# Kernel optimization log

Measured on AMD Instinct MI355X. Metric: run time of the kernel, lower is better.

Reference implementation:

```python
import jax, jax.numpy as jnp
import numpy as np

V, N = 3, 32768
C2, C3 = 256, 32          # feat_ch_2D, feat_ch_3D
H = W = 128               # 2D feature map size
D = 32                    # 3D volume feature size
CIN = C2 + C3             # 288, MLP in_channels


def setup_inputs() -> dict:
    key = jax.random.key(0)
    ks = jax.random.split(key, 16)
    sc = 0.02
    inp = {
        'pts': jax.random.uniform(ks[0], (1, N, 3), minval=-0.5, maxval=0.5),
        'pts_proj': jax.random.uniform(ks[1], (1, N, 2), minval=-1.0, maxval=1.0),
        'img_feat0': jax.random.normal(ks[2], (V, C2, H, W)),
        'img_feat1': jax.random.normal(ks[3], (V, C2, H, W)),
        'vol_feat0': jax.random.normal(ks[4], (V, C3, D, D, D)),
        'vol_feat1': jax.random.normal(ks[5], (V, C3, D, D, D)),
        'W0': jax.random.normal(ks[6], (1024, CIN)) * sc,  'b0': jnp.zeros((1024,)),
        'W1': jax.random.normal(ks[7], (512, CIN + 1024)) * sc, 'b1': jnp.zeros((512,)),
        'W2': jax.random.normal(ks[8], (256, CIN + 512)) * sc,  'b2': jnp.zeros((256,)),
        'W3': jax.random.normal(ks[9], (128, CIN + 256)) * sc,  'b3': jnp.zeros((128,)),
        'W4': jax.random.normal(ks[10], (1, 128)) * sc,         'b4': jnp.zeros((1,)),
        'mean_num': 3,
    }
    return inp


def _gs2d(feat, gx, gy):
    # feat: [C,H,W]; gx,gy: [N] normalized coords in [-1,1]
    C, Hh, Ww = feat.shape
    ix = jnp.clip(((gx + 1.0) * Ww - 1.0) * 0.5, 0.0, Ww - 1.0)  # align_corners=False, border pad
    iy = jnp.clip(((gy + 1.0) * Hh - 1.0) * 0.5, 0.0, Hh - 1.0)
    x0f, y0f = jnp.floor(ix), jnp.floor(iy)
    wx, wy = ix - x0f, iy - y0f
    x0 = x0f.astype(jnp.int32); x1 = jnp.minimum(x0 + 1, Ww - 1)
    y0 = y0f.astype(jnp.int32); y1 = jnp.minimum(y0 + 1, Hh - 1)
    v00 = feat[:, y0, x0]; v01 = feat[:, y0, x1]
    v10 = feat[:, y1, x0]; v11 = feat[:, y1, x1]
    return (v00 * (1 - wy) * (1 - wx) + v01 * (1 - wy) * wx
            + v10 * wy * (1 - wx) + v11 * wy * wx)  # [C,N]


def _gs3d(feat, gx, gy, gz):
    # feat: [C,D,H,W]; grid x->W, y->H, z->D (torch grid_sample convention)
    C, Dd, Hh, Ww = feat.shape
    ix = jnp.clip(((gx + 1.0) * Ww - 1.0) * 0.5, 0.0, Ww - 1.0)
    iy = jnp.clip(((gy + 1.0) * Hh - 1.0) * 0.5, 0.0, Hh - 1.0)
    iz = jnp.clip(((gz + 1.0) * Dd - 1.0) * 0.5, 0.0, Dd - 1.0)
    x0f, y0f, z0f = jnp.floor(ix), jnp.floor(iy), jnp.floor(iz)
    wx, wy, wz = ix - x0f, iy - y0f, iz - z0f
    x0 = x0f.astype(jnp.int32); x1 = jnp.minimum(x0 + 1, Ww - 1)
    y0 = y0f.astype(jnp.int32); y1 = jnp.minimum(y0 + 1, Hh - 1)
    z0 = z0f.astype(jnp.int32); z1 = jnp.minimum(z0 + 1, Dd - 1)
    def g(zi, yi, xi):
        return feat[:, zi, yi, xi]  # [C,N]
    out = (g(z0, y0, x0) * (1 - wz) * (1 - wy) * (1 - wx)
           + g(z0, y0, x1) * (1 - wz) * (1 - wy) * wx
           + g(z0, y1, x0) * (1 - wz) * wy * (1 - wx)
           + g(z0, y1, x1) * (1 - wz) * wy * wx
           + g(z1, y0, x0) * wz * (1 - wy) * (1 - wx)
           + g(z1, y0, x1) * wz * (1 - wy) * wx
           + g(z1, y1, x0) * wz * wy * (1 - wx)
           + g(z1, y1, x1) * wz * wy * wx)
    return out  # [C,N]


def _lrelu(x):
    return jnp.where(x >= 0, x, 0.2 * x)


def _conv1x1(Wm, bm, x):
    # x: [V,C,N] -> [V,O,N]
    return jnp.einsum('oc,vcn->von', Wm, x) + bm[None, :, None]


def _mlp0(x, W0, b0, W1, b1, W2, b2, W3, b3):
    out = _lrelu(_conv1x1(W0, b0, x))
    out = _lrelu(_conv1x1(W1, b1, jnp.concatenate([x, out], axis=1)))
    out = _lrelu(_conv1x1(W2, b2, jnp.concatenate([x, out], axis=1)))
    out = _lrelu(_conv1x1(W3, b3, jnp.concatenate([x, out], axis=1)))
    return out  # [V,128,N]


def _forward(pts, pts_proj, img_feats, vol_feats,
             W0, b0, W1, b1, W2, b2, W3, b3, W4, b4, mean_num):
    v = img_feats[0].shape[0]
    gx2 = jnp.broadcast_to(pts_proj[:, :, 0], (v, pts_proj.shape[1]))
    gy2 = jnp.broadcast_to(pts_proj[:, :, 1], (v, pts_proj.shape[1]))
    p = pts * 2.0  # pts *= 2.0 before 3D sampling
    gx3 = jnp.broadcast_to(p[:, :, 0], (v, p.shape[1]))
    gy3 = jnp.broadcast_to(p[:, :, 1], (v, p.shape[1]))
    gz3 = jnp.broadcast_to(p[:, :, 2], (v, p.shape[1]))
    outs = []
    for img_feat, vol_feat in zip(img_feats, vol_feats):
        f2 = jax.vmap(_gs2d)(img_feat, gx2, gy2)            # [V,C2,N]
        f3 = jax.vmap(_gs3d)(vol_feat, gx3, gy3, gz3)       # [V,C3,N]
        pt_feat = jnp.concatenate([f2, f3], axis=1)         # [V,288,N]
        pt_out0 = _mlp0(pt_feat, W0, b0, W1, b1, W2, b2, W3, b3)
        pt_out0_mean = jnp.mean(pt_out0[:mean_num], axis=0, keepdims=True)  # [1,128,N]
        sdf = jax.nn.sigmoid(_conv1x1(W4, b4, pt_out0_mean))                # [1,1,N]
        outs.append(jnp.transpose(sdf, (0, 2, 1)))                          # [1,N,1]
    return tuple(outs)


def reference(pts, pts_proj, img_feat0, img_feat1, vol_feat0, vol_feat1,
              W0, b0, W1, b1, W2, b2, W3, b3, W4, b4, mean_num):
    return _forward(pts, pts_proj, [img_feat0, img_feat1], [vol_feat0, vol_feat1],
                    W0, b0, W1, b1, W2, b2, W3, b3, W4, b4, mean_num)
```

## Files before the change

### kernel.cpp

```cpp
#include <hip/hip_runtime.h>
#include <hip/hip_bf16.h>

#define NV 3
#define NPTS 32768
#define C2C 256
#define C3C 32
#define CINC 288
#define HH 128
#define WWW 128
#define DDD 32

typedef short bh8 __attribute__((ext_vector_type(8)));
typedef float fx4 __attribute__((ext_vector_type(4)));
typedef unsigned short us4 __attribute__((ext_vector_type(4)));

__device__ __forceinline__ float b2f(unsigned short u) {
    unsigned int x = ((unsigned int)u) << 16;
    return __uint_as_float(x);
}
__device__ __forceinline__ unsigned short f2b(float f) {
    unsigned int x = __float_as_uint(f);
    unsigned int r = (x + 0x7FFFu + ((x >> 16) & 1u)) >> 16;
    return (unsigned short)r;
}

__device__ __forceinline__ void gl2lds16(const unsigned short* g, unsigned short* l) {
    __builtin_amdgcn_global_load_lds(
        (const __attribute__((address_space(1))) unsigned int*)g,
        (__attribute__((address_space(3))) unsigned int*)l, 16, 0, 0);
}

__global__ void k_f2b(const float* __restrict__ src, unsigned short* __restrict__ dst, int n) {
    int i = blockIdx.x * 256 + threadIdx.x;
    if (i < n) dst[i] = f2b(src[i]);
}

__global__ void k_timg(const float* __restrict__ in, unsigned short* __restrict__ out) {
    int v = blockIdx.x >> 7, y = blockIdx.x & 127;
    int x0 = blockIdx.y << 6, c0 = blockIdx.z << 6;
    __shared__ float t[64][65];
    int tx = threadIdx.x & 63, tg = threadIdx.x >> 6;
    const float* src = in + (((size_t)(v * C2C + c0) * HH + y) * WWW + x0);
#pragma unroll
    for (int i = 0; i < 16; i++) {
        int cl = tg * 16 + i;
        t[cl][tx] = src[(size_t)cl * (HH * WWW) + tx];
    }
    __syncthreads();
    unsigned short* dst = out + ((size_t)(v * HH + y) * WWW + x0) * C2C + c0;
#pragma unroll
    for (int i = 0; i < 16; i++) {
        int xl = tg * 16 + i;
        dst[(size_t)xl * C2C + tx] = f2b(t[tx][xl]);
    }
}

__global__ void k_tvol(const float* __restrict__ in, unsigned short* __restrict__ out) {
    int v = blockIdx.x;
    int s0 = blockIdx.y << 8;
    __shared__ float t[32][257];
    int tid = threadIdx.x;
    const float* src = in + (size_t)v * C3C * 32768 + s0;
#pragma unroll
    for (int c = 0; c < 32; c++) t[c][tid] = src[(size_t)c * 32768 + tid];
    __syncthreads();
    unsigned short* dst = out + ((size_t)v * 32768 + s0) * C3C;
    int c = tid & 31, sb = tid >> 5;
#pragma unroll
    for (int j = 0; j < 32; j++) {
        int sl = j * 8 + sb;
        dst[(size_t)sl * C3C + c] = f2b(t[c][sl]);
    }
}

__global__ __launch_bounds__(256) void k_sample(const float* __restrict__ pts, const float* __restrict__ proj,
                         const unsigned short* __restrict__ imgT, const unsigned short* __restrict__ volT,
                         unsigned short* __restrict__ ptT, int n0, int Nk) {
    int w = threadIdx.x >> 6, l = threadIdx.x & 63;
    int i = blockIdx.x * 4 + w;
    int v = blockIdx.y;
    int n = n0 + i;
    unsigned short* dstRow = ptT + (size_t)(v * Nk + i) * CINC;

    {
        float gx = proj[n * 2 + 0], gy = proj[n * 2 + 1];
        float ix = fminf(fmaxf(((gx + 1.0f) * (float)WWW - 1.0f) * 0.5f, 0.0f), (float)(WWW - 1));
        float iy = fminf(fmaxf(((gy + 1.0f) * (float)HH - 1.0f) * 0.5f, 0.0f), (float)(HH - 1));
        float x0f = floorf(ix), y0f = floorf(iy);
        float wx = ix - x0f, wy = iy - y0f;
        int x0 = (int)x0f, y0 = (int)y0f;
        int x1 = min(x0 + 1, WWW - 1), y1 = min(y0 + 1, HH - 1);
        const unsigned short* base = imgT + (size_t)v * HH * WWW * C2C;
        const us4* p00 = (const us4*)(base + ((size_t)(y0 * WWW + x0)) * C2C) + l;
        const us4* p01 = (const us4*)(base + ((size_t)(y0 * WWW + x1)) * C2C) + l;
        const us4* p10 = (const us4*)(base + ((size_t)(y1 * WWW + x0)) * C2C) + l;
        const us4* p11 = (const us4*)(base + ((size_t)(y1 * WWW + x1)) * C2C) + l;
        us4 a = *p00, b = *p01, c = *p10, d = *p11;
        float w00 = (1.0f - wy) * (1.0f - wx), w01 = (1.0f - wy) * wx;
        float w10 = wy * (1.0f - wx), w11 = wy * wx;
        us4 rv;
#pragma unroll
        for (int r = 0; r < 4; r++) {
            float f = b2f(a[r]) * w00 + b2f(b[r]) * w01 + b2f(c[r]) * w10 + b2f(d[r]) * w11;
            rv[r] = f2b(f);
        }
        *(us4*)(dstRow + l * 4) = rv;
    }
    {
        float gx = pts[n * 3 + 0] * 2.0f, gy = pts[n * 3 + 1] * 2.0f, gz = pts[n * 3 + 2] * 2.0f;
        float ix = fminf(fmaxf(((gx + 1.0f) * (float)DDD - 1.0f) * 0.5f, 0.0f), (float)(DDD - 1));
        float iy = fminf(fmaxf(((gy + 1.0f) * (float)DDD - 1.0f) * 0.5f, 0.0f), (float)(DDD - 1));
        float iz = fminf(fmaxf(((gz + 1.0f) * (float)DDD - 1.0f) * 0.5f, 0.0f), (float)(DDD - 1));
        float x0f = floorf(ix), y0f = floorf(iy), z0f = floorf(iz);
        float wx = ix - x0f, wy = iy - y0f, wz = iz - z0f;
        int x0 = (int)x0f, y0 = (int)y0f, z0 = (int)z0f;
        int x1 = min(x0 + 1, DDD - 1), y1 = min(y0 + 1, DDD - 1), z1 = min(z0 + 1, DDD - 1);
        int c = l & 31, zs = l >> 5;
        int zi = zs ? z1 : z0;
        float wzs = zs ? wz : (1.0f - wz);
        const unsigned short* base = volT + (size_t)v * 32768 * C3C;
        float f00 = b2f(base[((size_t)((zi * 32 + y0) * 32 + x0)) * C3C + c]);
        float f01 = b2f(base[((size_t)((zi * 32 + y0) * 32 + x1)) * C3C + c]);
        float f10 = b2f(base[((size_t)((zi * 32 + y1) * 32 + x0)) * C3C + c]);
        float f11 = b2f(base[((size_t)((zi * 32 + y1) * 32 + x1)) * C3C + c]);
        float r = (f00 * (1.0f - wy) * (1.0f - wx) + f01 * (1.0f - wy) * wx +
                   f10 * wy * (1.0f - wx) + f11 * wy * wx) * wzs;
        float other = __shfl_xor(r, 32);
        r += other;
        if (zs == 0) dstRow[C2C + c] = f2b(r);
    }
}

__global__ __launch_bounds__(256) void k_gemm(const unsigned short* __restrict__ A, int K,
                                              const unsigned short* __restrict__ B1, int K1,
                                              const unsigned short* __restrict__ B2, int K2,
                                              const float* __restrict__ bias,
                                              unsigned short* __restrict__ C, int M) {
    __shared__ unsigned short As[128 * 32];
    __shared__ unsigned short Bs[128 * 32];
    int tid = threadIdx.x;
    int w = tid >> 6, l = tid & 63;
    int la = l & 15, lg = l >> 4;
    int wm = w & 1, wn = w >> 1;
    int mBlk = blockIdx.x * 128;
    int nBlk = blockIdx.y * 128;

    int sRow = l >> 2;
    int sCol = (l & 3) * 8;

    fx4 acc[4][4];
#pragma unroll
    for (int mi = 0; mi < 4; mi++)
#pragma unroll
        for (int ni = 0; ni < 4; ni++) acc[mi][ni] = (fx4){0.f, 0.f, 0.f, 0.f};

    const unsigned short* Ag = A + (size_t)mBlk * K;
    const unsigned short* Bg;

#define KLOOP(BPTR, KB, AOFF)                                                                  \
    Bg = (BPTR) + (size_t)nBlk * (KB);                                                         \
    for (int k0 = 0; k0 < (KB); k0 += 32) {                                                    \
        _Pragma("unroll")                                                                      \
        for (int j = 0; j < 2; j++) {                                                          \
            int r = w * 32 + j * 16 + sRow;                                                    \
            gl2lds16(Ag + (size_t)r * K + (AOFF) + k0 + sCol, &As[r * 32 + sCol]);             \
            gl2lds16(Bg + (size_t)r * (KB) + k0 + sCol, &Bs[r * 32 + sCol]);                   \
        }                                                                                      \
        __syncthreads();                                                                       \
        bh8 af[4], bf8[4];                                                                     \
        _Pragma("unroll")                                                                      \
        for (int mi = 0; mi < 4; mi++) af[mi] = *(const bh8*)&As[(wm * 64 + mi * 16 + la) * 32 + lg * 8]; \
        _Pragma("unroll")                                                                      \
        for (int ni = 0; ni < 4; ni++) bf8[ni] = *(const bh8*)&Bs[(wn * 64 + ni * 16 + la) * 32 + lg * 8]; \
        _Pragma("unroll")                                                                      \
        for (int mi = 0; mi < 4; mi++)                                                         \
            _Pragma("unroll")                                                                  \
            for (int ni = 0; ni < 4; ni++)                                                     \
                acc[mi][ni] = __builtin_amdgcn_mfma_f32_16x16x32_bf16(af[mi], bf8[ni], acc[mi][ni], 0, 0, 0); \
        __syncthreads();                                                                       \
    }

    KLOOP(B1, K1, 0)
    if (B2 != nullptr) {
        KLOOP(B2, K2, K1)
    }
#undef KLOOP

#pragma unroll
    for (int mi = 0; mi < 4; mi++) {
        int m0 = mBlk + wm * 64 + mi * 16 + lg * 4;
        fx4 bb = *(const fx4*)(bias + m0);
#pragma unroll
        for (int ni = 0; ni < 4; ni++) {
            int n = nBlk + wn * 64 + ni * 16 + la;
            us4 rv;
#pragma unroll
            for (int r = 0; r < 4; r++) {
                float x = acc[mi][ni][r] + bb[r];
                x = (x >= 0.0f) ? x : 0.2f * x;
                rv[r] = f2b(x);
            }
            *(us4*)(C + (size_t)n * M + m0) = rv;
        }
    }
}

__global__ void k_head(const unsigned short* __restrict__ o3, const float* __restrict__ W4,
                       const float* __restrict__ b4, const int* __restrict__ mn_p,
                       float* __restrict__ out, int n0, int Nk, int level) {
    int i = blockIdx.x * 256 + threadIdx.x;
    if (i >= Nk) return;
    int mn = *mn_p;
    if (mn > NV) mn = NV;
    if (mn < 1) mn = 1;
    float s = 0.0f;
    for (int v = 0; v < mn; v++) {
        const unsigned short* row = o3 + (size_t)(v * Nk + i) * 128;
        for (int c0 = 0; c0 < 128; c0 += 8) {
            bh8 x = *(const bh8*)(row + c0);
#pragma unroll
            for (int r = 0; r < 8; r++) s += W4[c0 + r] * b2f((unsigned short)x[r]);
        }
    }
    s = s / (float)mn + b4[0];
    out[(size_t)level * NPTS + n0 + i] = 1.0f / (1.0f + expf(-s));
}

extern "C" void kernel_launch(void* const* d_in, const int* in_sizes, int n_in,
                              void* d_out, int out_size, void* d_ws, size_t ws_size,
                              hipStream_t stream) {
    const float* pts = (const float*)d_in[0];
    const float* proj = (const float*)d_in[1];
    const float* img[2] = {(const float*)d_in[2], (const float*)d_in[3]};
    const float* vol[2] = {(const float*)d_in[4], (const float*)d_in[5]};
    const float* Wf[4] = {(const float*)d_in[6], (const float*)d_in[8], (const float*)d_in[10], (const float*)d_in[12]};
    const float* bf[4] = {(const float*)d_in[7], (const float*)d_in[9], (const float*)d_in[11], (const float*)d_in[13]};
    const float* W4 = (const float*)d_in[14];
    const float* b4 = (const float*)d_in[15];
    const int* mn = (const int*)d_in[16];
    float* out = (float*)d_out;

    const int Ksz[4] = {288, 1312, 800, 544};
    const int Msz[4] = {1024, 512, 256, 128};

    char* ws = (char*)d_ws;
    size_t off = 0;
    auto alloc = [&](size_t bytes) -> char* {
        char* p = ws + off;
        off = (off + bytes + 255) & ~(size_t)255;
        return p;
    };

    unsigned short* Wb[4];
    for (int i = 0; i < 4; i++) Wb[i] = (unsigned short*)alloc((size_t)Msz[i] * Ksz[i] * 2);
    unsigned short* imgT = (unsigned short*)alloc((size_t)NV * HH * WWW * C2C * 2);
    unsigned short* volT = (unsigned short*)alloc((size_t)NV * 32768 * C3C * 2);
    size_t fixed = off;

    const size_t perPt = (size_t)NV * 2 * (CINC + 1024 + 512 + 256 + 128);
    int Nk = NPTS;
    if (fixed + (size_t)Nk * perPt + 4096 > ws_size) {
        size_t avail = (ws_size > fixed + 4096) ? (ws_size - fixed - 4096) : 0;
        long nk = (long)(avail / perPt);
        nk = (nk / 128) * 128;
        if (nk < 128) nk = 128;
        if (nk > NPTS) nk = NPTS;
        Nk = (int)nk;
    }
    unsigned short* ptT = (unsigned short*)alloc((size_t)NV * Nk * CINC * 2);
    unsigned short* o0 = (unsigned short*)alloc((size_t)NV * Nk * 1024 * 2);
    unsigned short* o1 = (unsigned short*)alloc((size_t)NV * Nk * 512 * 2);
    unsigned short* o2 = (unsigned short*)alloc((size_t)NV * Nk * 256 * 2);
    unsigned short* o3 = (unsigned short*)alloc((size_t)NV * Nk * 128 * 2);

    for (int i = 0; i < 4; i++) {
        int n = Msz[i] * Ksz[i];
        k_f2b<<<(n + 255) / 256, 256, 0, stream>>>(Wf[i], Wb[i], n);
    }

    for (int lvl = 0; lvl < 2; lvl++) {
        k_timg<<<dim3(NV * HH, WWW / 64, C2C / 64), 256, 0, stream>>>(img[lvl], imgT);
        k_tvol<<<dim3(NV, 32768 / 256), 256, 0, stream>>>(vol[lvl], volT);
        for (int n0 = 0; n0 < NPTS; n0 += Nk) {
            int nk = NPTS - n0 < Nk ? NPTS - n0 : Nk;
            int NC = NV * nk;
            k_sample<<<dim3(nk / 4, NV), 256, 0, stream>>>(pts, proj, imgT, volT, ptT, n0, nk);
            k_gemm<<<dim3(1024 / 128, NC / 128), 256, 0, stream>>>(Wb[0], 288, ptT, 288, nullptr, 0, bf[0], o0, 1024);
            k_gemm<<<dim3(512 / 128, NC / 128), 256, 0, stream>>>(Wb[1], 1312, ptT, 288, o0, 1024, bf[1], o1, 512);
            k_gemm<<<dim3(256 / 128, NC / 128), 256, 0, stream>>>(Wb[2], 800, ptT, 288, o1, 512, bf[2], o2, 256);
            k_gemm<<<dim3(128 / 128, NC / 128), 256, 0, stream>>>(Wb[3], 544, ptT, 288, o2, 256, bf[3], o3, 128);
            k_head<<<(nk + 255) / 256, 256, 0, stream>>>(o3, W4, b4, mn, out, n0, nk, lvl);
        }
    }
}
```

Baseline: 1.186 ms.

## Double-buffer GEMM LDS tiles and swizzle workgroups across XCDs

The GEMM kernel now uses two LDS buffers, so loads for the next K-tile are issued before computing on the current one. This halves the barriers per tile and overlaps global-to-LDS transfer with MFMA work. It also remaps block IDs so consecutive tiles land on the same XCD, which should improve L2 reuse. The cost is doubled LDS use per block, which may reduce occupancy.

New measurement: 1.209 ms. About the same (+2.0%).

```diff
diff --git a/kernel.cpp b/kernel.cpp
--- a/kernel.cpp
+++ b/kernel.cpp
@@ -28,6 +28,13 @@
     __builtin_amdgcn_global_load_lds(
         (const __attribute__((address_space(1))) unsigned int*)g,
         (__attribute__((address_space(3))) unsigned int*)l, 16, 0, 0);
+}
+
+__device__ __forceinline__ int xcd_swz(int orig, int nwg) {
+    int xcd = orig & 7;
+    int q = nwg >> 3, r = nwg & 7;
+    int base = (xcd < r) ? xcd * (q + 1) : r * (q + 1) + (xcd - r) * q;
+    return base + (orig >> 3);
 }
 
 __global__ void k_f2b(const float* __restrict__ src, unsigned short* __restrict__ dst, int n) {
@@ -91,11 +98,10 @@
         int x0 = (int)x0f, y0 = (int)y0f;
         int x1 = min(x0 + 1, WWW - 1), y1 = min(y0 + 1, HH - 1);
         const unsigned short* base = imgT + (size_t)v * HH * WWW * C2C;
-        const us4* p00 = (const us4*)(base + ((size_t)(y0 * WWW + x0)) * C2C) + l;
-        const us4* p01 = (const us4*)(base + ((size_t)(y0 * WWW + x1)) * C2C) + l;
-        const us4* p10 = (const us4*)(base + ((size_t)(y1 * WWW + x0)) * C2C) + l;
-        const us4* p11 = (const us4*)(base + ((size_t)(y1 * WWW + x1)) * C2C) + l;
-        us4 a = *p00, b = *p01, c = *p10, d = *p11;
+        us4 a = *((const us4*)(base + ((size_t)(y0 * WWW + x0)) * C2C) + l);
+        us4 b = *((const us4*)(base + ((size_t)(y0 * WWW + x1)) * C2C) + l);
+        us4 c = *((const us4*)(base + ((size_t)(y1 * WWW + x0)) * C2C) + l);
+        us4 d = *((const us4*)(base + ((size_t)(y1 * WWW + x1)) * C2C) + l);
         float w00 = (1.0f - wy) * (1.0f - wx), w01 = (1.0f - wy) * wx;
         float w10 = wy * (1.0f - wx), w11 = wy * wx;
         us4 rv;
@@ -136,17 +142,24 @@
                                               const unsigned short* __restrict__ B2, int K2,
                                               const float* __restrict__ bias,
                                               unsigned short* __restrict__ C, int M) {
-    __shared__ unsigned short As[128 * 32];
-    __shared__ unsigned short Bs[128 * 32];
+    __shared__ unsigned short As0[128 * 32], Bs0[128 * 32];
+    __shared__ unsigned short As1[128 * 32], Bs1[128 * 32];
     int tid = threadIdx.x;
     int w = tid >> 6, l = tid & 63;
     int la = l & 15, lg = l >> 4;
     int wm = w & 1, wn = w >> 1;
-    int mBlk = blockIdx.x * 128;
-    int nBlk = blockIdx.y * 128;
-
-    int sRow = l >> 2;
-    int sCol = (l & 3) * 8;
+    int gx = gridDim.x;
+    int nwg = gx * gridDim.y;
+    int bid = xcd_swz(blockIdx.y * gx + blockIdx.x, nwg);
+    int mBlk = (bid % gx) * 128;
+    int nBlk = (bid / gx) * 128;
+    int sRow = l >> 2, sCol = (l & 3) * 8;
+    int r0 = w * 32 + sRow, r1 = r0 + 16;
+
+    const unsigned short* Ag = A + (size_t)mBlk * K;
+    const unsigned short* B1g = B1 + (size_t)nBlk * K1;
+    const unsigned short* B2g = B2 ? B2 + (size_t)nBlk * K2 : (const unsigned short*)0;
+    int nt1 = K1 >> 5, nt = nt1 + (K2 >> 5);
 
     fx4 acc[4][4];
 #pragma unroll
@@ -154,37 +167,42 @@
 #pragma unroll
         for (int ni = 0; ni < 4; ni++) acc[mi][ni] = (fx4){0.f, 0.f, 0.f, 0.f};
 
-    const unsigned short* Ag = A + (size_t)mBlk * K;
-    const unsigned short* Bg;
-
-#define KLOOP(BPTR, KB, AOFF)                                                                  \
-    Bg = (BPTR) + (size_t)nBlk * (KB);                                                         \
-    for (int k0 = 0; k0 < (KB); k0 += 32) {                                                    \
-        _Pragma("unroll")                                                                      \
-        for (int j = 0; j < 2; j++) {                                                          \
-            int r = w * 32 + j * 16 + sRow;                                                    \
-            gl2lds16(Ag + (size_t)r * K + (AOFF) + k0 + sCol, &As[r * 32 + sCol]);             \
-            gl2lds16(Bg + (size_t)r * (KB) + k0 + sCol, &Bs[r * 32 + sCol]);                   \
-        }                                                                                      \
-        __syncthreads();                                                                       \
-        bh8 af[4], bf8[4];                                                                     \
-        _Pragma("unroll")                                                                      \
-        for (int mi = 0; mi < 4; mi++) af[mi] = *(const bh8*)&As[(wm * 64 + mi * 16 + la) * 32 + lg * 8]; \
-        _Pragma("unroll")                                                                      \
-        for (int ni = 0; ni < 4; ni++) bf8[ni] = *(const bh8*)&Bs[(wn * 64 + ni * 16 + la) * 32 + lg * 8]; \
-        _Pragma("unroll")                                                                      \
-        for (int mi = 0; mi < 4; mi++)                                                         \
-            _Pragma("unroll")                                                                  \
-            for (int ni = 0; ni < 4; ni++)                                                     \
-                acc[mi][ni] = __builtin_amdgcn_mfma_f32_16x16x32_bf16(af[mi], bf8[ni], acc[mi][ni], 0, 0, 0); \
-        __syncthreads();                                                                       \
-    }
-
-    KLOOP(B1, K1, 0)
-    if (B2 != nullptr) {
-        KLOOP(B2, K2, K1)
-    }
-#undef KLOOP
+    auto stage = [&](int t, unsigned short* Asb, unsigned short* Bsb) {
+        const unsigned short* as = Ag + t * 32 + sCol;
+        gl2lds16(as + (size_t)r0 * K, Asb + r0 * 32 + sCol);
+        gl2lds16(as + (size_t)r1 * K, Asb + r1 * 32 + sCol);
+        const unsigned short* bs;
+        size_t ldb;
+        if (t < nt1) { bs = B1g + t * 32 + sCol; ldb = (size_t)K1; }
+        else         { bs = B2g + (t - nt1) * 32 + sCol; ldb = (size_t)K2; }
+        gl2lds16(bs + (size_t)r0 * ldb, Bsb + r0 * 32 + sCol);
+        gl2lds16(bs + (size_t)r1 * ldb, Bsb + r1 * 32 + sCol);
+    };
+    auto compute = [&](const unsigned short* Asb, const unsigned short* Bsb) {
+        bh8 af[4], bf8[4];
+#pragma unroll
+        for (int mi = 0; mi < 4; mi++) af[mi] = *(const bh8*)&Asb[(wm * 64 + mi * 16 + la) * 32 + lg * 8];
+#pragma unroll
+        for (int ni = 0; ni < 4; ni++) bf8[ni] = *(const bh8*)&Bsb[(wn * 64 + ni * 16 + la) * 32 + lg * 8];
+#pragma unroll
+        for (int mi = 0; mi < 4; mi++)
+#pragma unroll
+            for (int ni = 0; ni < 4; ni++)
+                acc[mi][ni] = __builtin_amdgcn_mfma_f32_16x16x32_bf16(af[mi], bf8[ni], acc[mi][ni], 0, 0, 0);
+    };
+
+    stage(0, As0, Bs0);
+    __syncthreads();
+    for (int t = 0; t < nt; t += 2) {
+        if (t + 1 < nt) stage(t + 1, As1, Bs1);
+        compute(As0, Bs0);
+        __syncthreads();
+        if (t + 1 < nt) {
+            if (t + 2 < nt) stage(t + 2, As0, Bs0);
+            compute(As1, Bs1);
+            __syncthreads();
+        }
+    }
 
 #pragma unroll
     for (int mi = 0; mi < 4; mi++) {
```

## Add 256x256 double-buffered swizzled GEMM with padded K and XCD-aware block mapping

Applied to the files above, without the earlier changes.

Adds a new 512-thread GEMM kernel with 256x256 tiles, 64-wide K steps and double-buffered LDS. LDS loads use an XOR swizzle, waits use explicit vmcnt counts, and the MFMA sections are raised with setprio. The point features and weights are zero-padded from 288 to 320 columns so every K chunk is 64-aligned, and block ids are remapped across XCDs for better L2 locality. The first three MLP layers use the new kernel and the last keeps the old one with padded strides. The cost is extra padding work and much higher LDS and register use per block, which can limit occupancy.

New measurement: 1.183 ms. No clear change (-0.3%).

```diff
diff --git a/kernel.cpp b/kernel.cpp
--- a/kernel.cpp
+++ b/kernel.cpp
@@ -6,6 +6,7 @@
 #define C2C 256
 #define C3C 32
 #define CINC 288
+#define CINP 320
 #define HH 128
 #define WWW 128
 #define DDD 32
@@ -30,9 +31,23 @@
         (__attribute__((address_space(3))) unsigned int*)l, 16, 0, 0);
 }
 
-__global__ void k_f2b(const float* __restrict__ src, unsigned short* __restrict__ dst, int n) {
-    int i = blockIdx.x * 256 + threadIdx.x;
-    if (i < n) dst[i] = f2b(src[i]);
+__device__ __forceinline__ int xcd_swz(int orig, int nwg) {
+    int xcd = orig & 7;
+    int q = nwg >> 3, r = nwg & 7;
+    int base = (xcd < r) ? xcd * (q + 1) : r * (q + 1) + (xcd - r) * q;
+    return base + (orig >> 3);
+}
+
+__global__ void k_wpad(const float* __restrict__ src, unsigned short* __restrict__ dst, int M, int Kp) {
+    int idx = blockIdx.x * 256 + threadIdx.x;
+    if (idx >= M * Kp) return;
+    int m = idx / Kp, k = idx - m * Kp;
+    int Ksrc = Kp - 32;
+    float v;
+    if (k < CINC) v = src[(size_t)m * Ksrc + k];
+    else if (k < CINP) v = 0.0f;
+    else v = src[(size_t)m * Ksrc + (k - 32)];
+    dst[idx] = f2b(v);
 }
 
 __global__ void k_timg(const float* __restrict__ in, unsigned short* __restrict__ out) {
@@ -80,7 +95,7 @@
     int i = blockIdx.x * 4 + w;
     int v = blockIdx.y;
     int n = n0 + i;
-    unsigned short* dstRow = ptT + (size_t)(v * Nk + i) * CINC;
+    unsigned short* dstRow = ptT + (size_t)(v * Nk + i) * CINP;
 
     {
         float gx = proj[n * 2 + 0], gy = proj[n * 2 + 1];
@@ -91,11 +106,10 @@
         int x0 = (int)x0f, y0 = (int)y0f;
         int x1 = min(x0 + 1, WWW - 1), y1 = min(y0 + 1, HH - 1);
         const unsigned short* base = imgT + (size_t)v * HH * WWW * C2C;
-        const us4* p00 = (const us4*)(base + ((size_t)(y0 * WWW + x0)) * C2C) + l;
-        const us4* p01 = (const us4*)(base + ((size_t)(y0 * WWW + x1)) * C2C) + l;
-        const us4* p10 = (const us4*)(base + ((size_t)(y1 * WWW + x0)) * C2C) + l;
-        const us4* p11 = (const us4*)(base + ((size_t)(y1 * WWW + x1)) * C2C) + l;
-        us4 a = *p00, b = *p01, c = *p10, d = *p11;
+        us4 a = *((const us4*)(base + ((size_t)(y0 * WWW + x0)) * C2C) + l);
+        us4 b = *((const us4*)(base + ((size_t)(y0 * WWW + x1)) * C2C) + l);
+        us4 c = *((const us4*)(base + ((size_t)(y1 * WWW + x0)) * C2C) + l);
+        us4 d = *((const us4*)(base + ((size_t)(y1 * WWW + x1)) * C2C) + l);
         float w00 = (1.0f - wy) * (1.0f - wx), w01 = (1.0f - wy) * wx;
         float w10 = wy * (1.0f - wx), w11 = wy * wx;
         us4 rv;
@@ -129,6 +143,133 @@
         r += other;
         if (zs == 0) dstRow[C2C + c] = f2b(r);
     }
+    if (l < 8) *(us4*)(dstRow + CINC + l * 4) = (us4){0, 0, 0, 0};
+}
+
+__global__ __launch_bounds__(512) void k_gemm8(const unsigned short* __restrict__ A, int Kp,
+                                               const unsigned short* __restrict__ B1,
+                                               const unsigned short* __restrict__ B2, int K2,
+                                               const float* __restrict__ bias,
+                                               unsigned short* __restrict__ C, int M) {
+    __shared__ unsigned short As[2][256 * 64];
+    __shared__ unsigned short Bs[2][256 * 64];
+    int tid = threadIdx.x;
+    int w = tid >> 6, l = tid & 63;
+    int la = l & 15, lg = l >> 4;
+    int wm = w >> 2, wn = w & 3;
+    int g = wn >> 1;
+    int gx = gridDim.x;
+    int nwg = gx * gridDim.y;
+    int bid = xcd_swz(blockIdx.y * gx + blockIdx.x, nwg);
+    int mBlk = (bid % gx) * 256;
+    int nBlk = (bid / gx) * 256;
+    int nt = Kp >> 6;
+
+    const unsigned short* Ag = A + (size_t)mBlk * Kp;
+
+    fx4 acc[8][4];
+#pragma unroll
+    for (int mi = 0; mi < 8; mi++)
+#pragma unroll
+        for (int ni = 0; ni < 4; ni++) acc[mi][ni] = (fx4){0.f, 0.f, 0.f, 0.f};
+
+    auto burst = [&](int t, int nxt) {
+        const unsigned short* bsrc;
+        size_t ldb;
+        int kc;
+        if (t < 5) { bsrc = B1; ldb = CINP; kc = t * 64; }
+        else       { bsrc = B2; ldb = (size_t)K2; kc = (t - 5) * 64; }
+        bsrc += (size_t)nBlk * ldb + kc;
+        const unsigned short* asrc = Ag + t * 64;
+#pragma unroll
+        for (int h = 0; h < 2; h++)
+#pragma unroll
+            for (int j = 0; j < 2; j++) {
+                int idx = j * 512 + tid;
+                int r = (h << 7) + (idx >> 3);
+                int c = (idx & 7) ^ (r & 7);
+                gl2lds16(asrc + (size_t)r * Kp + c * 8, &As[nxt][(h << 13) + idx * 8]);
+            }
+#pragma unroll
+        for (int h = 0; h < 2; h++)
+#pragma unroll
+            for (int j = 0; j < 2; j++) {
+                int idx = j * 512 + tid;
+                int r = (h << 7) + (idx >> 3);
+                int c = (idx & 7) ^ (r & 7);
+                gl2lds16(bsrc + (size_t)r * ldb + c * 8, &Bs[nxt][(h << 13) + idx * 8]);
+            }
+    };
+
+    burst(0, 0);
+    for (int t = 0; t < nt; t++) {
+        int cur = t & 1;
+        if (t + 1 < nt) {
+            burst(t + 1, cur ^ 1);
+            if (g == 0) asm volatile("s_waitcnt vmcnt(10)" ::: "memory");
+            else        asm volatile("s_waitcnt vmcnt(8)" ::: "memory");
+        } else {
+            if (g == 0) asm volatile("s_waitcnt vmcnt(2)" ::: "memory");
+            else        asm volatile("s_waitcnt vmcnt(0)" ::: "memory");
+        }
+        const unsigned short* Ab = &As[cur][0];
+        const unsigned short* Bb = &Bs[cur][0];
+        bh8 afr[4][2];
+#pragma unroll
+        for (int p = 0; p < 4; p++) {
+            int qm = p >> 1, qn = p & 1;
+            if (qn == 0) {
+#pragma unroll
+                for (int m2 = 0; m2 < 4; m2++)
+#pragma unroll
+                    for (int s = 0; s < 2; s++) {
+                        int row = wm * 128 + (qm * 4 + m2) * 16 + la;
+                        int c = (s * 4 + lg) ^ (row & 7);
+                        afr[m2][s] = *(const bh8*)&Ab[row * 64 + c * 8];
+                    }
+            }
+            bh8 bfr[2][2];
+#pragma unroll
+            for (int n2 = 0; n2 < 2; n2++)
+#pragma unroll
+                for (int s = 0; s < 2; s++) {
+                    int row = wn * 64 + (qn * 2 + n2) * 16 + la;
+                    int c = (s * 4 + lg) ^ (row & 7);
+                    bfr[n2][s] = *(const bh8*)&Bb[row * 64 + c * 8];
+                }
+            __builtin_amdgcn_s_barrier();
+            __builtin_amdgcn_s_setprio(1);
+#pragma unroll
+            for (int m2 = 0; m2 < 4; m2++)
+#pragma unroll
+                for (int n2 = 0; n2 < 2; n2++)
+#pragma unroll
+                    for (int s = 0; s < 2; s++)
+                        acc[qm * 4 + m2][qn * 2 + n2] = __builtin_amdgcn_mfma_f32_16x16x32_bf16(
+                            afr[m2][s], bfr[n2][s], acc[qm * 4 + m2][qn * 2 + n2], 0, 0, 0);
+            __builtin_amdgcn_s_setprio(0);
+            if (p == 3) asm volatile("s_waitcnt lgkmcnt(0)" ::: "memory");
+            __builtin_amdgcn_s_barrier();
+        }
+    }
+
+#pragma unroll
+    for (int mi = 0; mi < 8; mi++) {
+        int m0 = mBlk + wm * 128 + mi * 16 + lg * 4;
+        fx4 bb = *(const fx4*)(bias + m0);
+#pragma unroll
+        for (int ni = 0; ni < 4; ni++) {
+            int n = nBlk + wn * 64 + ni * 16 + la;
+            us4 rv;
+#pragma unroll
+            for (int r = 0; r < 4; r++) {
+                float x = acc[mi][ni][r] + bb[r];
+                x = (x >= 0.0f) ? x : 0.2f * x;
+                rv[r] = f2b(x);
+            }
+            *(us4*)(C + (size_t)n * M + m0) = rv;
+        }
+    }
 }
 
 __global__ __launch_bounds__(256) void k_gemm(const unsigned short* __restrict__ A, int K,
@@ -136,14 +277,17 @@
                                               const unsigned short* __restrict__ B2, int K2,
                                               const float* __restrict__ bias,
                                               unsigned short* __restrict__ C, int M) {
-    __shared__ unsigned short As[128 * 32];
-    __shared__ unsigned short Bs[128 * 32];
+    __shared__ unsigned short Ash[128 * 32];
+    __shared__ unsigned short Bsh[128 * 32];
     int tid = threadIdx.x;
     int w = tid >> 6, l = tid & 63;
     int la = l & 15, lg = l >> 4;
     int wm = w & 1, wn = w >> 1;
-    int mBlk = blockIdx.x * 128;
-    int nBlk = blockIdx.y * 128;
+    int gx = gridDim.x;
+    int nwg = gx * gridDim.y;
+    int bid = xcd_swz(blockIdx.y * gx + blockIdx.x, nwg);
+    int mBlk = (bid % gx) * 128;
+    int nBlk = (bid / gx) * 128;
 
     int sRow = l >> 2;
     int sCol = (l & 3) * 8;
@@ -163,20 +307,20 @@
         _Pragma("unroll")                                                                      \
         for (int j = 0; j < 2; j++) {                                                          \
             int r = w * 32 + j * 16 + sRow;                                                    \
-            gl2lds16(Ag + (size_t)r * K + (AOFF) + k0 + sCol, &As[r * 32 + sCol]);             \
-            gl2lds16(Bg + (size_t)r * (KB) + k0 + sCol, &Bs[r * 32 + sCol]);                   \
+            gl2lds16(Ag + (size_t)r * K + (AOFF) + k0 + sCol, &Ash[r * 32 + sCol]);            \
+            gl2lds16(Bg + (size_t)r * (KB) + k0 + sCol, &Bsh[r * 32 + sCol]);                  \
         }                                                                                      \
         __syncthreads();                                                                       \
-        bh8 af[4], bf8[4];                                                                     \
+        bh8 af[4], bfv[4];                                                                     \
         _Pragma("unroll")                                                                      \
-        for (int mi = 0; mi < 4; mi++) af[mi] = *(const bh8*)&As[(wm * 64 + mi * 16 + la) * 32 + lg * 8]; \
+        for (int mi = 0; mi < 4; mi++) af[mi] = *(const bh8*)&Ash[(wm * 64 + mi * 16 + la) * 32 + lg * 8]; \
         _Pragma("unroll")                                                                      \
-        for (int ni = 0; ni < 4; ni++) bf8[ni] = *(const bh8*)&Bs[(wn * 64 + ni * 16 + la) * 32 + lg * 8]; \
+        for (int ni = 0; ni < 4; ni++) bfv[ni] = *(const bh8*)&Bsh[(wn * 64 + ni * 16 + la) * 32 + lg * 8]; \
         _Pragma("unroll")                                                                      \
         for (int mi = 0; mi < 4; mi++)                                                         \
             _Pragma("unroll")                                                                  \
             for (int ni = 0; ni < 4; ni++)                                                     \
-                acc[mi][ni] = __builtin_amdgcn_mfma_f32_16x16x32_bf16(af[mi], bf8[ni], acc[mi][ni], 0, 0, 0); \
+                acc[mi][ni] = __builtin_amdgcn_mfma_f32_16x16x32_bf16(af[mi], bfv[ni], acc[mi][ni], 0, 0, 0); \
         __syncthreads();                                                                       \
     }
 
@@ -240,7 +384,7 @@
     const int* mn = (const int*)d_in[16];
     float* out = (float*)d_out;
 
-    const int Ksz[4] = {288, 1312, 800, 544};
+    const int Kp[4] = {320, 1344, 832, 576};
     const int Msz[4] = {1024, 512, 256, 128};
 
     char* ws = (char*)d_ws;
@@ -252,30 +396,30 @@
     };
 
     unsigned short* Wb[4];
-    for (int i = 0; i < 4; i++) Wb[i] = (unsigned short*)alloc((size_t)Msz[i] * Ksz[i] * 2);
+    for (int i = 0; i < 4; i++) Wb[i] = (unsigned short*)alloc((size_t)Msz[i] * Kp[i] * 2);
     unsigned short* imgT = (unsigned short*)alloc((size_t)NV * HH * WWW * C2C * 2);
     unsigned short* volT = (unsigned short*)alloc((size_t)NV * 32768 * C3C * 2);
     size_t fixed = off;
 
-    const size_t perPt = (size_t)NV * 2 * (CINC + 1024 + 512 + 256 + 128);
+    const size_t perPt = (size_t)NV * 2 * (CINP + 1024 + 512 + 256 + 128);
     int Nk = NPTS;
     if (fixed + (size_t)Nk * perPt + 4096 > ws_size) {
         size_t avail = (ws_size > fixed + 4096) ? (ws_size - fixed - 4096) : 0;
         long nk = (long)(avail / perPt);
-        nk = (nk / 128) * 128;
-        if (nk < 128) nk = 128;
+        nk = (nk / 256) * 256;
+        if (nk < 256) nk = 256;
         if (nk > NPTS) nk = NPTS;
         Nk = (int)nk;
     }
-    unsigned short* ptT = (unsigned short*)alloc((size_t)NV * Nk * CINC * 2);
+    unsigned short* ptT = (unsigned short*)alloc((size_t)NV * Nk * CINP * 2);
     unsigned short* o0 = (unsigned short*)alloc((size_t)NV * Nk * 1024 * 2);
     unsigned short* o1 = (unsigned short*)alloc((size_t)NV * Nk * 512 * 2);
     unsigned short* o2 = (unsigned short*)alloc((size_t)NV * Nk * 256 * 2);
     unsigned short* o3 = (unsigned short*)alloc((size_t)NV * Nk * 128 * 2);
 
     for (int i = 0; i < 4; i++) {
-        int n = Msz[i] * Ksz[i];
-        k_f2b<<<(n + 255) / 256, 256, 0, stream>>>(Wf[i], Wb[i], n);
+        int n = Msz[i] * Kp[i];
+        k_wpad<<<(n + 255) / 256, 256, 0, stream>>>(Wf[i], Wb[i], Msz[i], Kp[i]);
     }
 
     for (int lvl = 0; lvl < 2; lvl++) {
@@ -285,10 +429,10 @@
             int nk = NPTS - n0 < Nk ? NPTS - n0 : Nk;
             int NC = NV * nk;
             k_sample<<<dim3(nk / 4, NV), 256, 0, stream>>>(pts, proj, imgT, volT, ptT, n0, nk);
-            k_gemm<<<dim3(1024 / 128, NC / 128), 256, 0, stream>>>(Wb[0], 288, ptT, 288, nullptr, 0, bf[0], o0, 1024);
-            k_gemm<<<dim3(512 / 128, NC / 128), 256, 0, stream>>>(Wb[1], 1312, ptT, 288, o0, 1024, bf[1], o1, 512);
-            k_gemm<<<dim3(256 / 128, NC / 128), 256, 0, stream>>>(Wb[2], 800, ptT, 288, o1, 512, bf[2], o2, 256);
-            k_gemm<<<dim3(128 / 128, NC / 128), 256, 0, stream>>>(Wb[3], 544, ptT, 288, o2, 256, bf[3], o3, 128);
+            k_gemm8<<<dim3(1024 / 256, NC / 256), 512, 0, stream>>>(Wb[0], Kp[0], ptT, nullptr, 0, bf[0], o0, 1024);
+            k_gemm8<<<dim3(512 / 256, NC / 256), 512, 0, stream>>>(Wb[1], Kp[1], ptT, o0, 1024, bf[1], o1, 512);
+            k_gemm8<<<dim3(256 / 256, NC / 256), 512, 0, stream>>>(Wb[2], Kp[2], ptT, o1, 512, bf[2], o2, 256);
+            k_gemm<<<dim3(128 / 128, NC / 128), 256, 0, stream>>>(Wb[3], Kp[3], ptT, CINP, o2, 256, bf[3], o3, 128);
             k_head<<<(nk + 255) / 256, 256, 0, stream>>>(o3, W4, b4, mn, out, n0, nk, lvl);
         }
     }
```
